# Performance work log

Hardware: AMD Instinct MI355X
Metric: run time of the kernel (lower is better)

## Reference

```python
import jax, jax.numpy as jnp
import numpy as np

B, T, D, ACT, H = 4096, 128, 64, 2, 64

def setup_inputs() -> dict:
    key = jax.random.key(0)
    ks = jax.random.split(key, 8)
    s = 1.0 / np.sqrt(H)
    return {
        "s0": jax.random.normal(ks[0], (B, D), jnp.float32),
        "a": jax.random.normal(ks[1], (B, T, ACT), jnp.float32),
        "w_ih": jax.random.uniform(ks[2], (3 * H, D + ACT), jnp.float32, -s, s),
        "w_hh": jax.random.uniform(ks[3], (3 * H, H), jnp.float32, -s, s),
        "b_ih": jax.random.uniform(ks[4], (3 * H,), jnp.float32, -s, s),
        "b_hh": jax.random.uniform(ks[5], (3 * H,), jnp.float32, -s, s),
        "w_out": jax.random.uniform(ks[6], (D, H), jnp.float32, -s, s),
        "b_out": jax.random.uniform(ks[7], (D,), jnp.float32, -s, s),
    }

def reference(s0, a, w_ih, w_hh, b_ih, b_hh, w_out, b_out):
    # PyTorch GRUCell convention: gates ordered (r, z, n)
    h0 = jnp.zeros((s0.shape[0], w_hh.shape[1]), s0.dtype)

    def step(carry, a_t):
        h, s = carry
        x = jnp.concatenate([s, a_t], axis=-1)              # [B, D+ACT]
        gi = x @ w_ih.T + b_ih                              # [B, 3H]
        gh = h @ w_hh.T + b_hh                              # [B, 3H]
        i_r, i_z, i_n = jnp.split(gi, 3, axis=-1)
        h_r, h_z, h_n = jnp.split(gh, 3, axis=-1)
        r = jax.nn.sigmoid(i_r + h_r)
        z = jax.nn.sigmoid(i_z + h_z)
        n = jnp.tanh(i_n + r * h_n)
        h_new = (1.0 - z) * n + z * h
        s_new = h_new @ w_out.T + b_out                     # [B, D]
        return (h_new, s_new), s_new

    a_tbd = jnp.swapaxes(a, 0, 1)                           # [T, B, ACT]
    _, outs = jax.lax.scan(step, (h0, s0), a_tbd)           # outs: [T, B, D]
    return jnp.swapaxes(outs, 0, 1)                         # [B, T, D]
```

## Files before the change

### kernel.cpp

```cpp
#include <hip/hip_runtime.h>
#include <hip/hip_bf16.h>

typedef __attribute__((ext_vector_type(8))) short bf16x8;
typedef __attribute__((ext_vector_type(4))) float f32x4;
typedef __attribute__((ext_vector_type(2))) float f32x2;

typedef bf16x8 bf16x8_a __attribute__((may_alias));
typedef f32x4  f32x4_a  __attribute__((may_alias));
typedef f32x2  f32x2_a  __attribute__((may_alias));
typedef unsigned short u16a __attribute__((may_alias));
typedef unsigned int u32;

__device__ __forceinline__ float fexp2(float x) {
  float r; asm("v_exp_f32 %0, %1" : "=v"(r) : "v"(x)); return r;
}
__device__ __forceinline__ float frcp(float x) {
  float r; asm("v_rcp_f32 %0, %1" : "=v"(r) : "v"(x)); return r;
}
__device__ __forceinline__ float sigf(float x) {
  return frcp(1.f + fexp2(x * -1.44269504f));
}
__device__ __forceinline__ float tanhf_(float x) {
  return 1.f - 2.f * frcp(1.f + fexp2(x * 2.88539008f));
}
__device__ __forceinline__ u32 cvtpk(float lo, float hi) {
  u32 r; asm("v_cvt_pk_bf16_f32 %0, %1, %2" : "=v"(r) : "v"(lo), "v"(hi)); return r;
}

#define LDS_WG   0
#define LDS_HB   24576
#define LDS_SIZE 28672

__device__ __forceinline__ void stbf(char* smem, int byteoff, float v) {
  union { __hip_bfloat16 b; unsigned short u; } cv;
  cv.b = __float2bfloat16(v);
  *(u16a*)(smem + byteoff) = cv.u;
}
__device__ __forceinline__ void st16(char* smem, int byteoff, unsigned short v) {
  *(u16a*)(smem + byteoff) = v;
}

__device__ __forceinline__ bf16x8 packf8(const float* v) {
  bf16x8 r;
  #pragma unroll
  for (int j = 0; j < 8; ++j) {
    union { __hip_bfloat16 b; short u; } cv;
    cv.b = __float2bfloat16(v[j]);
    r[j] = cv.u;
  }
  return r;
}

__device__ __forceinline__ void xbar() {
  asm volatile("s_waitcnt lgkmcnt(0)\n\ts_barrier" ::: "memory");
}

__global__ __launch_bounds__(256, 1)
void gru_fused(const float* __restrict__ s0, const float* __restrict__ a,
               const float* __restrict__ w_ih, const float* __restrict__ w_hh,
               const float* __restrict__ b_ih, const float* __restrict__ b_hh,
               const float* __restrict__ w_out, const float* __restrict__ b_out,
               float* __restrict__ out)
{
  __shared__ __align__(16) char smem[LDS_SIZE];
  const int tid = threadIdx.x;
  const int l = tid & 63;
  const int w = tid >> 6;
  const int c = l & 15;
  const int g = l >> 4;
  const int b0 = blockIdx.x * 16;
  const int swzc = (c & 7) << 4;

  for (int idx = tid; idx < 16 * 64; idx += 256) {
    int r = idx >> 6, k = idx & 63;
    stbf(smem, LDS_HB + r * 128 + ((k * 2) ^ ((r & 7) << 4)), s0[(b0 + r) * 64 + k]);
  }

  bf16x8 bwo[4][2];
  #pragma unroll
  for (int i = 0; i < 4; ++i) {
    #pragma unroll
    for (int ks = 0; ks < 2; ++ks) {
      float tv[8];
      #pragma unroll
      for (int j = 0; j < 8; ++j)
        tv[j] = w_out[(ks * 32 + g * 8 + j) * 64 + c + 16 * i];
      bwo[i][ks] = packf8(tv);
    }
  }
  #pragma unroll
  for (int rr = 0; rr < 3; ++rr) {
    int rt = w + 4 * rr;
    bf16x8 wsa[2];
    #pragma unroll
    for (int ks = 0; ks < 2; ++ks) {
      float tv[8];
      #pragma unroll
      for (int u = 0; u < 4; ++u) {
        f32x2 t2 = *(const f32x2_a*)(w_ih + (16 * rt + c) * 66 + ks * 32 + g * 8 + 2 * u);
        tv[2 * u] = t2.x; tv[2 * u + 1] = t2.y;
      }
      wsa[ks] = packf8(tv);
    }
    f32x4 acc[4];
    #pragma unroll
    for (int i = 0; i < 4; ++i) {
      #pragma unroll
      for (int j = 0; j < 4; ++j) {
        int n = 16 * rt + 4 * g + j;
        acc[i][j] = (n < 128) ? w_hh[n * 64 + c + 16 * i] : 0.f;
      }
    }
    #pragma unroll
    for (int i = 0; i < 4; ++i)
      #pragma unroll
      for (int ks = 0; ks < 2; ++ks)
        acc[i] = __builtin_amdgcn_mfma_f32_16x16x32_bf16(wsa[ks], bwo[i][ks], acc[i], 0, 0, 0);
    #pragma unroll
    for (int i = 0; i < 4; ++i)
      #pragma unroll
      for (int j = 0; j < 4; ++j) {
        int n = 16 * rt + 4 * g + j;
        stbf(smem, LDS_WG + n * 128 + (((c + 16 * i) * 2) ^ ((n & 7) << 4)), acc[i][j]);
      }
  }

  const int nr = 16 * w + c, nz = 64 + nr, ni = 128 + nr;
  float bs_r = 0.f, bs_z = 0.f, bs_i = 0.f;
  for (int d = 0; d < 64; ++d) {
    float bo = b_out[d];
    bs_r += w_ih[nr * 66 + d] * bo;
    bs_z += w_ih[nz * 66 + d] * bo;
    bs_i += w_ih[ni * 66 + d] * bo;
  }
  const float wa0_r = w_ih[nr * 66 + 64], wa1_r = w_ih[nr * 66 + 65];
  const float wa0_z = w_ih[nz * 66 + 64], wa1_z = w_ih[nz * 66 + 65];
  const float wa0_i = w_ih[ni * 66 + 64], wa1_i = w_ih[ni * 66 + 65];
  const float pb_r = b_ih[nr] + b_hh[nr];
  const float pb_z = b_ih[nz] + b_hh[nz];
  const float pb_i = b_ih[ni];
  const float bias_r = pb_r + bs_r;
  const float bias_z = pb_z + bs_z;
  const float bias_i = pb_i + bs_i;
  const float bias_hn = b_hh[ni];
  const float bias_o = b_out[nr];

  bf16x8 whn[2], wo[2], wsr[2], wsz[2], wsi[2];
  #pragma unroll
  for (int ks = 0; ks < 2; ++ks) {
    float tv[8];
    f32x4 t4;
    t4 = *(const f32x4_a*)(w_hh + ni * 64 + ks * 32 + g * 8);
    tv[0] = t4.x; tv[1] = t4.y; tv[2] = t4.z; tv[3] = t4.w;
    t4 = *(const f32x4_a*)(w_hh + ni * 64 + ks * 32 + g * 8 + 4);
    tv[4] = t4.x; tv[5] = t4.y; tv[6] = t4.z; tv[7] = t4.w;
    whn[ks] = packf8(tv);
    t4 = *(const f32x4_a*)(w_out + nr * 64 + ks * 32 + g * 8);
    tv[0] = t4.x; tv[1] = t4.y; tv[2] = t4.z; tv[3] = t4.w;
    t4 = *(const f32x4_a*)(w_out + nr * 64 + ks * 32 + g * 8 + 4);
    tv[4] = t4.x; tv[5] = t4.y; tv[6] = t4.z; tv[7] = t4.w;
    wo[ks] = packf8(tv);
    #pragma unroll
    for (int u = 0; u < 4; ++u) {
      f32x2 t2 = *(const f32x2_a*)(w_ih + nr * 66 + ks * 32 + g * 8 + 2 * u);
      tv[2 * u] = t2.x; tv[2 * u + 1] = t2.y;
    }
    wsr[ks] = packf8(tv);
    #pragma unroll
    for (int u = 0; u < 4; ++u) {
      f32x2 t2 = *(const f32x2_a*)(w_ih + nz * 66 + ks * 32 + g * 8 + 2 * u);
      tv[2 * u] = t2.x; tv[2 * u + 1] = t2.y;
    }
    wsz[ks] = packf8(tv);
    #pragma unroll
    for (int u = 0; u < 4; ++u) {
      f32x2 t2 = *(const f32x2_a*)(w_ih + ni * 66 + ks * 32 + g * 8 + 2 * u);
      tv[2 * u] = t2.x; tv[2 * u + 1] = t2.y;
    }
    wsi[ks] = packf8(tv);
  }

  int aoff[4], ooff[4];
  #pragma unroll
  for (int j = 0; j < 4; ++j) {
    int gr = b0 + 4 * g + j;
    aoff[j] = gr * 256;
    ooff[j] = gr * 8192 + nr;
  }

  __syncthreads();

  bf16x8 wgr[2], wgz[2], wgi[2];
  #pragma unroll
  for (int ks = 0; ks < 2; ++ks) {
    wgr[ks] = *(const bf16x8_a*)(smem + LDS_WG + nr * 128 + ((ks * 64 + g * 16) ^ swzc));
    wgz[ks] = *(const bf16x8_a*)(smem + LDS_WG + nz * 128 + ((ks * 64 + g * 16) ^ swzc));
    wgi[ks] = *(const bf16x8_a*)(smem + LDS_WG + ni * 128 + ((ks * 64 + g * 16) ^ swzc));
  }

  bf16x8 sa[2];
  #pragma unroll
  for (int ks = 0; ks < 2; ++ks)
    sa[ks] = *(const bf16x8_a*)(smem + LDS_HB + c * 128 + ((ks * 64 + g * 16) ^ swzc));
  f32x4 ar, az, ai;
  #pragma unroll
  for (int j = 0; j < 4; ++j) {
    f32x2 av = *(const f32x2_a*)(a + aoff[j]);
    ar[j] = pb_r + av.x * wa0_r + av.y * wa1_r;
    az[j] = pb_z + av.x * wa0_z + av.y * wa1_z;
    ai[j] = pb_i + av.x * wa0_i + av.y * wa1_i;
  }
  #pragma unroll
  for (int ks = 0; ks < 2; ++ks) {
    ar = __builtin_amdgcn_mfma_f32_16x16x32_bf16(sa[ks], wsr[ks], ar, 0, 0, 0);
    az = __builtin_amdgcn_mfma_f32_16x16x32_bf16(sa[ks], wsz[ks], az, 0, 0, 0);
    ai = __builtin_amdgcn_mfma_f32_16x16x32_bf16(sa[ks], wsi[ks], ai, 0, 0, 0);
  }
  float hreg[4];
  #pragma unroll
  for (int j = 0; j < 4; ++j) {
    float r = sigf(ar[j]);
    float z = sigf(az[j]);
    float nn = tanhf_(ai[j] + r * bias_hn);
    hreg[j] = nn - z * nn;
  }
  {
    u32 p01 = cvtpk(hreg[0], hreg[1]);
    u32 p23 = cvtpk(hreg[2], hreg[3]);
    int r0 = 4 * g;
    st16(smem, LDS_HB + 2048 + (r0    ) * 128 + ((2 * nr) ^ (((r0    ) & 7) << 4)), (unsigned short)(p01));
    st16(smem, LDS_HB + 2048 + (r0 + 1) * 128 + ((2 * nr) ^ (((r0 + 1) & 7) << 4)), (unsigned short)(p01 >> 16));
    st16(smem, LDS_HB + 2048 + (r0 + 2) * 128 + ((2 * nr) ^ (((r0 + 2) & 7) << 4)), (unsigned short)(p23));
    st16(smem, LDS_HB + 2048 + (r0 + 3) * 128 + ((2 * nr) ^ (((r0 + 3) & 7) << 4)), (unsigned short)(p23 >> 16));
  }
  f32x2 avn[4];
  #pragma unroll
  for (int j = 0; j < 4; ++j)
    avn[j] = *(const f32x2_a*)(a + 2 + aoff[j]);
  xbar();

  #pragma unroll 1
  for (int t = 1; t < 128; ++t) {
    const char* hb = smem + LDS_HB + (t & 1) * 2048 + c * 128;
    bf16x8 ha0 = *(const bf16x8_a*)(hb + ((g * 16) ^ swzc));
    bf16x8 ha1 = *(const bf16x8_a*)(hb + ((64 + g * 16) ^ swzc));

    f32x4 arr, azz, aii, ahh;
    #pragma unroll
    for (int j = 0; j < 4; ++j) {
      arr[j] = bias_r + avn[j].x * wa0_r + avn[j].y * wa1_r;
      azz[j] = bias_z + avn[j].x * wa0_z + avn[j].y * wa1_z;
      aii[j] = bias_i + avn[j].x * wa0_i + avn[j].y * wa1_i;
      ahh[j] = bias_hn;
    }
    {
      const float* apn = a + 2 * ((t < 127) ? (t + 1) : 127);
      #pragma unroll
      for (int j = 0; j < 4; ++j)
        avn[j] = *(const f32x2_a*)(apn + aoff[j]);
    }

    arr = __builtin_amdgcn_mfma_f32_16x16x32_bf16(ha0, wgr[0], arr, 0, 0, 0);
    arr = __builtin_amdgcn_mfma_f32_16x16x32_bf16(ha1, wgr[1], arr, 0, 0, 0);
    azz = __builtin_amdgcn_mfma_f32_16x16x32_bf16(ha0, wgz[0], azz, 0, 0, 0);
    azz = __builtin_amdgcn_mfma_f32_16x16x32_bf16(ha1, wgz[1], azz, 0, 0, 0);
    aii = __builtin_amdgcn_mfma_f32_16x16x32_bf16(ha0, wgi[0], aii, 0, 0, 0);
    aii = __builtin_amdgcn_mfma_f32_16x16x32_bf16(ha1, wgi[1], aii, 0, 0, 0);
    ahh = __builtin_amdgcn_mfma_f32_16x16x32_bf16(ha0, whn[0], ahh, 0, 0, 0);
    ahh = __builtin_amdgcn_mfma_f32_16x16x32_bf16(ha1, whn[1], ahh, 0, 0, 0);

    float hv[4];
    #pragma unroll
    for (int j = 0; j < 4; ++j) {
      float r = sigf(arr[j]);
      float z = sigf(azz[j]);
      float nn = tanhf_(aii[j] + r * ahh[j]);
      float h = nn + z * (hreg[j] - nn);
      hv[j] = h;
      hreg[j] = h;
    }
    {
      u32 p01 = cvtpk(hv[0], hv[1]);
      u32 p23 = cvtpk(hv[2], hv[3]);
      int r0 = 4 * g;
      char* hbn = smem + LDS_HB + ((t + 1) & 1) * 2048;
      st16(hbn, (r0    ) * 128 + ((2 * nr) ^ (((r0    ) & 7) << 4)), (unsigned short)(p01));
      st16(hbn, (r0 + 1) * 128 + ((2 * nr) ^ (((r0 + 1) & 7) << 4)), (unsigned short)(p01 >> 16));
      st16(hbn, (r0 + 2) * 128 + ((2 * nr) ^ (((r0 + 2) & 7) << 4)), (unsigned short)(p23));
      st16(hbn, (r0 + 3) * 128 + ((2 * nr) ^ (((r0 + 3) & 7) << 4)), (unsigned short)(p23 >> 16));
    }
    f32x4 ao = f32x4{bias_o, bias_o, bias_o, bias_o};
    ao = __builtin_amdgcn_mfma_f32_16x16x32_bf16(ha0, wo[0], ao, 0, 0, 0);
    ao = __builtin_amdgcn_mfma_f32_16x16x32_bf16(ha1, wo[1], ao, 0, 0, 0);
    {
      float* ob = out + (size_t)(t - 1) * 64;
      #pragma unroll
      for (int j = 0; j < 4; ++j)
        ob[ooff[j]] = ao[j];
    }
    xbar();
  }

  {
    const char* hb = smem + LDS_HB + 0 * 2048 + c * 128;
    bf16x8 ha0 = *(const bf16x8_a*)(hb + ((g * 16) ^ swzc));
    bf16x8 ha1 = *(const bf16x8_a*)(hb + ((64 + g * 16) ^ swzc));
    f32x4 ao = f32x4{bias_o, bias_o, bias_o, bias_o};
    ao = __builtin_amdgcn_mfma_f32_16x16x32_bf16(ha0, wo[0], ao, 0, 0, 0);
    ao = __builtin_amdgcn_mfma_f32_16x16x32_bf16(ha1, wo[1], ao, 0, 0, 0);
    float* ob = out + (size_t)127 * 64;
    #pragma unroll
    for (int j = 0; j < 4; ++j)
      ob[ooff[j]] = ao[j];
  }
}

extern "C" void kernel_launch(void* const* d_in, const int* in_sizes, int n_in,
                              void* d_out, int out_size, void* d_ws, size_t ws_size,
                              hipStream_t stream) {
  const float* s0    = (const float*)d_in[0];
  const float* a     = (const float*)d_in[1];
  const float* w_ih  = (const float*)d_in[2];
  const float* w_hh  = (const float*)d_in[3];
  const float* b_ih  = (const float*)d_in[4];
  const float* b_hh  = (const float*)d_in[5];
  const float* w_out = (const float*)d_in[6];
  const float* b_out = (const float*)d_in[7];
  float* out = (float*)d_out;
  hipLaunchKernelGGL(gru_fused, dim3(4096 / 16), dim3(256), 0, stream,
                     s0, a, w_ih, w_hh, b_ih, b_hh, w_out, b_out, out);
}
```

Baseline: 76.51 us.

## Halve batch rows per block and split gate elementwise work across half-waves

Each block now handles 8 batch rows instead of 16 and launches twice as many blocks, zero-padding the unused half of the MFMA tile. The MFMA outputs for the valid rows are redistributed with ds_bpermute, so each lane evaluates only two sigmoid/tanh triples instead of four. Launch bounds allow two blocks per CU. The aim is to shorten the serial per-step critical path (transcendental math) and raise occupancy, at the cost of half-wasted MFMA throughput and extra cross-lane permutes each step.

```diff
diff --git a/kernel.cpp b/kernel.cpp
--- a/kernel.cpp
+++ b/kernel.cpp
@@ -27,6 +27,11 @@
   u32 r; asm("v_cvt_pk_bf16_f32 %0, %1, %2" : "=v"(r) : "v"(lo), "v"(hi)); return r;
 }
 
+__device__ __forceinline__ float combine(float x, float y, int bpidx, bool lo32) {
+  float bp = __int_as_float(__builtin_amdgcn_ds_bpermute(bpidx, __float_as_int(y)));
+  return lo32 ? x : bp;
+}
+
 #define LDS_WG   0
 #define LDS_HB   24576
 #define LDS_SIZE 28672
@@ -55,7 +60,7 @@
   asm volatile("s_waitcnt lgkmcnt(0)\n\ts_barrier" ::: "memory");
 }
 
-__global__ __launch_bounds__(256, 1)
+__global__ __launch_bounds__(256, 2)
 void gru_fused(const float* __restrict__ s0, const float* __restrict__ a,
                const float* __restrict__ w_ih, const float* __restrict__ w_hh,
                const float* __restrict__ b_ih, const float* __restrict__ b_hh,
@@ -68,12 +73,14 @@
   const int w = tid >> 6;
   const int c = l & 15;
   const int g = l >> 4;
-  const int b0 = blockIdx.x * 16;
+  const int b0 = blockIdx.x * 8;
   const int swzc = (c & 7) << 4;
 
-  for (int idx = tid; idx < 16 * 64; idx += 256) {
-    int r = idx >> 6, k = idx & 63;
-    stbf(smem, LDS_HB + r * 128 + ((k * 2) ^ ((r & 7) << 4)), s0[(b0 + r) * 64 + k]);
+  for (int idx = tid; idx < 2 * 16 * 64; idx += 256) {
+    int buf = idx >> 10;
+    int r = (idx >> 6) & 15, k = idx & 63;
+    float v = (buf == 0 && r < 8) ? s0[(b0 + r) * 64 + k] : 0.f;
+    stbf(smem, LDS_HB + buf * 2048 + r * 128 + ((k * 2) ^ ((r & 7) << 4)), v);
   }
 
   bf16x8 bwo[4][2];
@@ -180,12 +187,16 @@
     wsi[ks] = packf8(tv);
   }
 
-  int aoff[4], ooff[4];
+  const int r0 = 4 * (g & 1) + 2 * (g >> 1);
+  const bool lo32 = (l < 32);
+  const int bpidx = (l ^ 32) << 2;
+  int aoffC[4], ooffC[4];
   #pragma unroll
   for (int j = 0; j < 4; ++j) {
-    int gr = b0 + 4 * g + j;
-    aoff[j] = gr * 256;
-    ooff[j] = gr * 8192 + nr;
+    int rj = 4 * g + j;
+    if (rj > 7) rj = 7;
+    aoffC[j] = (b0 + rj) * 256;
+    ooffC[j] = (b0 + rj) * 8192 + nr;
   }
 
   __syncthreads();
@@ -205,7 +216,7 @@
   f32x4 ar, az, ai;
   #pragma unroll
   for (int j = 0; j < 4; ++j) {
-    f32x2 av = *(const f32x2_a*)(a + aoff[j]);
+    f32x2 av = *(const f32x2_a*)(a + aoffC[j]);
     ar[j] = pb_r + av.x * wa0_r + av.y * wa1_r;
     az[j] = pb_z + av.x * wa0_z + av.y * wa1_z;
     ai[j] = pb_i + av.x * wa0_i + av.y * wa1_i;
@@ -216,27 +227,25 @@
     az = __builtin_amdgcn_mfma_f32_16x16x32_bf16(sa[ks], wsz[ks], az, 0, 0, 0);
     ai = __builtin_amdgcn_mfma_f32_16x16x32_bf16(sa[ks], wsi[ks], ai, 0, 0, 0);
   }
-  float hreg[4];
-  #pragma unroll
-  for (int j = 0; j < 4; ++j) {
-    float r = sigf(ar[j]);
-    float z = sigf(az[j]);
-    float nn = tanhf_(ai[j] + r * bias_hn);
-    hreg[j] = nn - z * nn;
-  }
+  float hreg0, hreg1;
   {
-    u32 p01 = cvtpk(hreg[0], hreg[1]);
-    u32 p23 = cvtpk(hreg[2], hreg[3]);
-    int r0 = 4 * g;
-    st16(smem, LDS_HB + 2048 + (r0    ) * 128 + ((2 * nr) ^ (((r0    ) & 7) << 4)), (unsigned short)(p01));
-    st16(smem, LDS_HB + 2048 + (r0 + 1) * 128 + ((2 * nr) ^ (((r0 + 1) & 7) << 4)), (unsigned short)(p01 >> 16));
-    st16(smem, LDS_HB + 2048 + (r0 + 2) * 128 + ((2 * nr) ^ (((r0 + 2) & 7) << 4)), (unsigned short)(p23));
-    st16(smem, LDS_HB + 2048 + (r0 + 3) * 128 + ((2 * nr) ^ (((r0 + 3) & 7) << 4)), (unsigned short)(p23 >> 16));
+    float er0 = combine(ar[0], ar[2], bpidx, lo32), er1 = combine(ar[1], ar[3], bpidx, lo32);
+    float ez0 = combine(az[0], az[2], bpidx, lo32), ez1 = combine(az[1], az[3], bpidx, lo32);
+    float ei0 = combine(ai[0], ai[2], bpidx, lo32), ei1 = combine(ai[1], ai[3], bpidx, lo32);
+    float r_0 = sigf(er0), r_1 = sigf(er1);
+    float z_0 = sigf(ez0), z_1 = sigf(ez1);
+    float n_0 = tanhf_(ei0 + r_0 * bias_hn);
+    float n_1 = tanhf_(ei1 + r_1 * bias_hn);
+    hreg0 = n_0 - z_0 * n_0;
+    hreg1 = n_1 - z_1 * n_1;
+    u32 p = cvtpk(hreg0, hreg1);
+    st16(smem, LDS_HB + 2048 + (r0    ) * 128 + ((2 * nr) ^ (((r0    ) & 7) << 4)), (unsigned short)(p));
+    st16(smem, LDS_HB + 2048 + (r0 + 1) * 128 + ((2 * nr) ^ (((r0 + 1) & 7) << 4)), (unsigned short)(p >> 16));
   }
   f32x2 avn[4];
   #pragma unroll
   for (int j = 0; j < 4; ++j)
-    avn[j] = *(const f32x2_a*)(a + 2 + aoff[j]);
+    avn[j] = *(const f32x2_a*)(a + 2 + aoffC[j]);
   xbar();
 
   #pragma unroll 1
@@ -257,7 +266,7 @@
       const float* apn = a + 2 * ((t < 127) ? (t + 1) : 127);
       #pragma unroll
       for (int j = 0; j < 4; ++j)
-        avn[j] = *(const f32x2_a*)(apn + aoff[j]);
+        avn[j] = *(const f32x2_a*)(apn + aoffC[j]);
     }
 
     arr = __builtin_amdgcn_mfma_f32_16x16x32_bf16(ha0, wgr[0], arr, 0, 0, 0);
@@ -269,34 +278,33 @@
     ahh = __builtin_amdgcn_mfma_f32_16x16x32_bf16(ha0, whn[0], ahh, 0, 0, 0);
     ahh = __builtin_amdgcn_mfma_f32_16x16x32_bf16(ha1, whn[1], ahh, 0, 0, 0);
 
-    float hv[4];
-    #pragma unroll
-    for (int j = 0; j < 4; ++j) {
-      float r = sigf(arr[j]);
-      float z = sigf(azz[j]);
-      float nn = tanhf_(aii[j] + r * ahh[j]);
-      float h = nn + z * (hreg[j] - nn);
-      hv[j] = h;
-      hreg[j] = h;
-    }
+    float er0 = combine(arr[0], arr[2], bpidx, lo32), er1 = combine(arr[1], arr[3], bpidx, lo32);
+    float ez0 = combine(azz[0], azz[2], bpidx, lo32), ez1 = combine(azz[1], azz[3], bpidx, lo32);
+    float ei0 = combine(aii[0], aii[2], bpidx, lo32), ei1 = combine(aii[1], aii[3], bpidx, lo32);
+    float eh0 = combine(ahh[0], ahh[2], bpidx, lo32), eh1 = combine(ahh[1], ahh[3], bpidx, lo32);
+
+    float r_0 = sigf(er0), r_1 = sigf(er1);
+    float z_0 = sigf(ez0), z_1 = sigf(ez1);
+    float n_0 = tanhf_(ei0 + r_0 * eh0);
+    float n_1 = tanhf_(ei1 + r_1 * eh1);
+    float hv0 = n_0 + z_0 * (hreg0 - n_0);
+    float hv1 = n_1 + z_1 * (hreg1 - n_1);
+    hreg0 = hv0; hreg1 = hv1;
+
     {
-      u32 p01 = cvtpk(hv[0], hv[1]);
-      u32 p23 = cvtpk(hv[2], hv[3]);
-      int r0 = 4 * g;
+      u32 p = cvtpk(hv0, hv1);
       char* hbn = smem + LDS_HB + ((t + 1) & 1) * 2048;
-      st16(hbn, (r0    ) * 128 + ((2 * nr) ^ (((r0    ) & 7) << 4)), (unsigned short)(p01));
-      st16(hbn, (r0 + 1) * 128 + ((2 * nr) ^ (((r0 + 1) & 7) << 4)), (unsigned short)(p01 >> 16));
-      st16(hbn, (r0 + 2) * 128 + ((2 * nr) ^ (((r0 + 2) & 7) << 4)), (unsigned short)(p23));
-      st16(hbn, (r0 + 3) * 128 + ((2 * nr) ^ (((r0 + 3) & 7) << 4)), (unsigned short)(p23 >> 16));
+      st16(hbn, (r0    ) * 128 + ((2 * nr) ^ (((r0    ) & 7) << 4)), (unsigned short)(p));
+      st16(hbn, (r0 + 1) * 128 + ((2 * nr) ^ (((r0 + 1) & 7) << 4)), (unsigned short)(p >> 16));
     }
     f32x4 ao = f32x4{bias_o, bias_o, bias_o, bias_o};
     ao = __builtin_amdgcn_mfma_f32_16x16x32_bf16(ha0, wo[0], ao, 0, 0, 0);
     ao = __builtin_amdgcn_mfma_f32_16x16x32_bf16(ha1, wo[1], ao, 0, 0, 0);
-    {
+    if (lo32) {
       float* ob = out + (size_t)(t - 1) * 64;
       #pragma unroll
       for (int j = 0; j < 4; ++j)
-        ob[ooff[j]] = ao[j];
+        ob[ooffC[j]] = ao[j];
     }
     xbar();
   }
@@ -308,10 +316,12 @@
     f32x4 ao = f32x4{bias_o, bias_o, bias_o, bias_o};
     ao = __builtin_amdgcn_mfma_f32_16x16x32_bf16(ha0, wo[0], ao, 0, 0, 0);
     ao = __builtin_amdgcn_mfma_f32_16x16x32_bf16(ha1, wo[1], ao, 0, 0, 0);
-    float* ob = out + (size_t)127 * 64;
-    #pragma unroll
-    for (int j = 0; j < 4; ++j)
-      ob[ooff[j]] = ao[j];
+    if (lo32) {
+      float* ob = out + (size_t)127 * 64;
+      #pragma unroll
+      for (int j = 0; j < 4; ++j)
+        ob[ooffC[j]] = ao[j];
+    }
   }
 }
 
@@ -327,6 +337,6 @@
   const float* w_out = (const float*)d_in[6];
   const float* b_out = (const float*)d_in[7];
   float* out = (float*)d_out;
-  hipLaunchKernelGGL(gru_fused, dim3(4096 / 16), dim3(256), 0, stream,
+  hipLaunchKernelGGL(gru_fused, dim3(4096 / 8), dim3(256), 0, stream,
                      s0, a, w_ih, w_hh, b_ih, b_hh, w_out, b_out, out);
 }
```

Result: slower. 99.65 us (+30.2%).
